# Performance work log

Hardware: AMD Instinct MI355X
Metric: run time of the kernel (lower is better)

Reference implementation:

```python
import jax, jax.numpy as jnp
import numpy as np

B, T, L, E, H, QS = 8, 8, 197, 768, 12, 16
C = E // H


def setup_inputs() -> dict:
    key = jax.random.key(0)
    ks = jax.random.split(key, 10)
    return dict(
        x=jax.random.normal(ks[0], (B, T, L, E), jnp.float32) * 0.02,
        s=jax.random.normal(ks[1], (B, QS, E), jnp.float32) * 0.02,
        te=jax.random.normal(ks[2], (T, E), jnp.float32) * 0.02,
        patch_mask=jax.random.normal(ks[3], (B, T, 1, L - 1, 1), jnp.float32) * 0.02,
        in_proj_weight=jax.random.normal(ks[4], (3 * E, E), jnp.float32) * 0.02,
        in_proj_bias=jax.random.normal(ks[5], (3 * E,), jnp.float32) * 0.02,
        out_w=jax.random.normal(ks[6], (E, E), jnp.float32) * 0.02,
        out_b=jax.random.normal(ks[7], (E,), jnp.float32) * 0.02,
        conv_w=jax.random.normal(ks[8], (E, 1, 3), jnp.float32) * 0.001,  # depthwise, groups=E
        conv_b=jax.random.normal(ks[9], (E,), jnp.float32) * 0.02,
    )


def _qkv(z, w, b, head_shape):
    # F.linear(z, w, b).chunk(3, -1), each reshaped to (*head_shape, H, C)
    zz = z @ w.T + b
    q, k, v = jnp.split(zz, 3, axis=-1)
    return (q.reshape(*head_shape, H, C),
            k.reshape(*head_shape, H, C),
            v.reshape(*head_shape, H, C))


def reference(x, s, te, patch_mask, in_proj_weight, in_proj_bias, out_w, out_b, conv_w, conv_b):
    scale = 1.0 / jnp.sqrt(jnp.asarray(C, x.dtype))

    # main self-attention over patches, per frame
    q, k, v = _qkv(x, in_proj_weight, in_proj_bias, (B, T, L))
    aff = jnp.einsum('ntqhc,ntkhc->ntqkh', q * scale, k)
    aff = jax.nn.softmax(aff, axis=-2)  # softmax over key dim (dim=-2)
    mix = jnp.einsum('ntqlh,ntlhc->ntqhc', aff, v)
    out = mix.reshape(B, T, L, E) @ out_w.T + out_b

    # syno cross-attention stream
    s_q, s_k, s_v = _qkv(s, in_proj_weight, in_proj_bias, (B, QS))
    te_q, te_k, te_v = _qkv(te, in_proj_weight, in_proj_bias, (T, 1))  # [T,1,H,C]
    _k = k[:, :, 1:]  # drop CLS -> [B,T,L-1,H,C]
    _v = v[:, :, 1:]
    s_aff = jnp.einsum('nqhc,ntkhc->ntqkh', s_q * scale, _k + te_k)
    s_aff = s_aff + patch_mask
    s_aff = jax.nn.softmax(s_aff, axis=-2)
    s_mix = jnp.einsum('ntqlh,ntlhc->ntqhc', s_aff, _v + te_v)  # [B,T,QS,H,C]

    # depthwise temporal conv (kernel 3, pad 1, groups=E) with residual
    sm = s_mix.transpose(0, 2, 3, 4, 1).reshape(B * QS, E, T)  # [N*Q, E, T]
    conv = jax.lax.conv_general_dilated(
        sm, conv_w, window_strides=(1,), padding=((1, 1),),
        feature_group_count=E, dimension_numbers=('NCH', 'OIH', 'NCH'))
    sm = conv + conv_b[None, :, None] + sm
    s_mix = sm.reshape(B, QS, H, C, T).transpose(0, 4, 1, 2, 3)  # [B,T,QS,H,C]

    s_mix = s_mix.mean(axis=1)  # mean over frames -> [B,QS,H,C]
    s_out = s_mix.reshape(B, QS, E) @ out_w.T + out_b

    return (q, k, v, out, s_q, s_k, s_v, s_out)
```

## Files before the change

kernel.cpp:

```cpp
#include <hip/hip_runtime.h>
#include <math.h>

constexpr int Bb  = 8;
constexpr int Tt  = 8;
constexpr int Ll  = 197;
constexpr int Ee  = 768;
constexpr int Hh  = 12;
constexpr int QSs = 16;
constexpr int Cc  = 64;
constexpr int MX    = Bb * Tt * Ll;
constexpr int MS    = Bb * QSs;
constexpr int MTE   = Tt;
constexpr int MPAD  = 12800;
constexpr int KkP = 224;

using f32x4 = __attribute__((ext_vector_type(4))) float;
using s16x8 = __attribute__((ext_vector_type(8))) short;

__device__ __forceinline__ unsigned short f2bf(float f) {
    unsigned int u = __float_as_uint(f);
    u = (u + 0x7fffu + ((u >> 16) & 1u)) >> 16;
    return (unsigned short)u;
}

__global__ __launch_bounds__(256) void convert_all(
    const float* __restrict__ x, const float* __restrict__ s,
    const float* __restrict__ te, const float* __restrict__ ipw,
    const float* __restrict__ ow, unsigned short* __restrict__ xb,
    unsigned short* __restrict__ wb, unsigned short* __restrict__ owb)
{
    const long oX  = (long)MX * Ee;
    const long oS  = oX + (long)MS * Ee;
    const long oTe = oS + (long)MTE * Ee;
    const long nXp = (long)MPAD * Ee;
    const long nW  = (long)3 * Ee * Ee;
    const long nOW = (long)Ee * Ee;
    const long i4 = ((long)blockIdx.x * 256 + threadIdx.x) * 4;

    const float* src = nullptr; unsigned short* dst; long off, soff = 0;
    if (i4 < nXp) {
        dst = xb; off = i4;
        if      (off < oX)  { src = x;  soff = off; }
        else if (off < oS)  { src = s;  soff = off - oX; }
        else if (off < oTe) { src = te; soff = off - oS; }
    } else if (i4 < nXp + nW) {
        dst = wb; off = i4 - nXp; src = ipw; soff = off;
    } else if (i4 < nXp + nW + nOW) {
        dst = owb; off = i4 - nXp - nW; src = ow; soff = off;
    } else return;

    float4 v = make_float4(0.f, 0.f, 0.f, 0.f);
    if (src) v = *reinterpret_cast<const float4*>(src + soff);
    ushort4 o;
    o.x = f2bf(v.x); o.y = f2bf(v.y); o.z = f2bf(v.z); o.w = f2bf(v.w);
    *reinterpret_cast<ushort4*>(dst + off) = o;
}

struct DstPtrs { float* d[9]; };

__device__ __forceinline__ void load_lds16(const unsigned short* g, unsigned short* l) {
    __builtin_amdgcn_global_load_lds(
        (const __attribute__((address_space(1))) unsigned int*)g,
        (__attribute__((address_space(3))) unsigned int*)l,
        16, 0, 0);
}

__global__ __launch_bounds__(1024, 4) void mfma_gemm256(
    const unsigned short* __restrict__ A,
    const unsigned short* __restrict__ W,
    const float* __restrict__ bias,
    DstPtrs dp, int Mmain, int Ms, int Mte,
    int ntiles, int tilesPerSeg)
{
    __shared__ __align__(16) unsigned short Asm[2][256 * 64];
    __shared__ __align__(16) unsigned short Bsm[2][256 * 64];

    const int nwg = gridDim.x;
    const int bid = blockIdx.x;
    const int q8 = nwg >> 3, r8 = nwg & 7;
    const int xcd = bid & 7, pos = bid >> 3;
    const int wgid = (xcd < r8 ? xcd * (q8 + 1)
                               : r8 * (q8 + 1) + (xcd - r8) * q8) + pos;
    const int mtile = wgid / ntiles;
    const int ntile = wgid - mtile * ntiles;

    const int tid  = threadIdx.x;
    const int wave = tid >> 6;
    const int lane = tid & 63;
    const int wm = wave >> 2;
    const int wn = wave & 3;
    const int m0  = mtile * 256;
    const int n0w = ntile * 256;
    const int seg = ntile / tilesPerSeg;
    const int n0g = (ntile % tilesPerSeg) * 256;

    const int frow = lane & 15;
    const int g    = lane >> 4;
    const int axr  = frow & 7;
    const int c0   = (g ^ axr) * 16;
    const int c1   = ((4 + g) ^ axr) * 16;

    f32x4 acc[4][4];
#pragma unroll
    for (int i = 0; i < 4; ++i)
#pragma unroll
        for (int j = 0; j < 4; ++j)
            acc[i][j] = f32x4{0.f, 0.f, 0.f, 0.f};

    const int srow = tid >> 3;
    const int scol = ((tid & 7) ^ ((tid >> 3) & 7)) * 8;
    const int sdst = tid * 8;

    const unsigned short* gA = A + (size_t)(m0 + srow) * 768 + scol;
    const unsigned short* gB = W + (size_t)(n0w + srow) * 768 + scol;

    auto STAGE_A = [&](int kt, int b) {
        const int k1 = kt * 64;
#pragma unroll
        for (int r = 0; r < 2; ++r)
            load_lds16(gA + (size_t)(r * 128) * 768 + k1,
                       &Asm[b][(r * 128) * 64 + sdst]);
    };
    auto STAGE_B = [&](int kt, int b) {
        const int k1 = kt * 64;
#pragma unroll
        for (int r = 0; r < 2; ++r)
            load_lds16(gB + (size_t)(r * 128) * 768 + k1,
                       &Bsm[b][(r * 128) * 64 + sdst]);
    };

    STAGE_A(0, 0);
    STAGE_B(0, 0);
    asm volatile("s_waitcnt vmcnt(0)" ::: "memory");
    __builtin_amdgcn_s_barrier();
    __builtin_amdgcn_sched_barrier(0);

    const int arow0 = wm * 64 + frow;
    const int brow0 = wn * 64 + frow;

    for (int kt = 0; kt < 12; ++kt) {
        const int cur = kt & 1;
        const char* As_ = (const char*)&Asm[cur][0];
        const char* Bs_ = (const char*)&Bsm[cur][0];
        const bool pre = kt < 11;

        s16x8 afr[4], bfr[4];
#pragma unroll
        for (int m = 0; m < 4; ++m)
            afr[m] = *reinterpret_cast<const s16x8*>(As_ + (arow0 + m * 16) * 128 + c0);
#pragma unroll
        for (int n = 0; n < 4; ++n)
            bfr[n] = *reinterpret_cast<const s16x8*>(Bs_ + (brow0 + n * 16) * 128 + c0);
        if (pre) { STAGE_A(kt + 1, cur ^ 1); STAGE_B(kt + 1, cur ^ 1); }
        asm volatile("s_waitcnt lgkmcnt(0)" ::: "memory");
        __builtin_amdgcn_sched_barrier(0);
        __builtin_amdgcn_s_setprio(1);
#pragma unroll
        for (int m = 0; m < 4; ++m)
#pragma unroll
            for (int n = 0; n < 4; ++n)
                acc[m][n] = __builtin_amdgcn_mfma_f32_16x16x32_bf16(
                    afr[m], bfr[n], acc[m][n], 0, 0, 0);
        __builtin_amdgcn_s_setprio(0);
#pragma unroll
        for (int m = 0; m < 4; ++m)
            afr[m] = *reinterpret_cast<const s16x8*>(As_ + (arow0 + m * 16) * 128 + c1);
#pragma unroll
        for (int n = 0; n < 4; ++n)
            bfr[n] = *reinterpret_cast<const s16x8*>(Bs_ + (brow0 + n * 16) * 128 + c1);
        asm volatile("s_waitcnt lgkmcnt(0)" ::: "memory");
        __builtin_amdgcn_sched_barrier(0);
        __builtin_amdgcn_s_setprio(1);
#pragma unroll
        for (int m = 0; m < 4; ++m)
#pragma unroll
            for (int n = 0; n < 4; ++n)
                acc[m][n] = __builtin_amdgcn_mfma_f32_16x16x32_bf16(
                    afr[m], bfr[n], acc[m][n], 0, 0, 0);
        __builtin_amdgcn_s_setprio(0);
        __builtin_amdgcn_sched_barrier(0);
        asm volatile("s_waitcnt vmcnt(0)" ::: "memory");
        __builtin_amdgcn_s_barrier();
        __builtin_amdgcn_sched_barrier(0);
    }

    {
        float* sc = (wave < 8 ? reinterpret_cast<float*>(&Asm[0][0])
                              : reinterpret_cast<float*>(&Bsm[0][0]))
                    + (wave & 7) * 1088;
        float bv[4];
#pragma unroll
        for (int n = 0; n < 4; ++n)
            bv[n] = bias[n0w + wn * 64 + n * 16 + frow];

        const int erow = lane >> 2;
        const int ecg  = lane & 3;

#pragma unroll
        for (int m = 0; m < 4; ++m) {
#pragma unroll
            for (int n = 0; n < 4; ++n)
#pragma unroll
                for (int r = 0; r < 4; ++r)
                    sc[(g * 4 + r) * 68 + n * 16 + frow] = acc[m][n][r] + bv[n];

            const int grow = m0 + wm * 64 + m * 16 + erow;
            float* base = nullptr; int lr = 0;
            if (grow < Mmain)                 { base = dp.d[seg];     lr = grow; }
            else if (grow < Mmain + Ms)       { base = dp.d[3 + seg]; lr = grow - Mmain; }
            else if (grow < Mmain + Ms + Mte) { base = dp.d[6 + seg]; lr = grow - Mmain - Ms; }
            if (base) {
                float* p = base + (size_t)lr * 768 + n0g + wn * 64 + ecg * 16;
                const float* sr = sc + erow * 68 + ecg * 16;
#pragma unroll
                for (int kq = 0; kq < 4; ++kq)
                    *reinterpret_cast<float4*>(p + kq * 4) =
                        *reinterpret_cast<const float4*>(sr + kq * 4);
            }
        }
    }
}

__global__ __launch_bounds__(256) void mfma_gemm(
    const unsigned short* __restrict__ A,
    const unsigned short* __restrict__ W,
    const float* __restrict__ bias,
    DstPtrs dp, int Mmain, int Ms, int Mte,
    int ntiles, int tilesPerSeg)
{
    __shared__ __align__(16) unsigned short Asm[2][128 * 32];
    __shared__ __align__(16) unsigned short Bsm[2][128 * 32];

    const int nwg = gridDim.x;
    const int bid = blockIdx.x;
    const int q8 = nwg >> 3, r8 = nwg & 7;
    const int xcd = bid & 7, pos = bid >> 3;
    const int wgid = (xcd < r8 ? xcd * (q8 + 1)
                               : r8 * (q8 + 1) + (xcd - r8) * q8) + pos;
    const int mtile = wgid / ntiles;
    const int ntile = wgid - mtile * ntiles;

    const int tid  = threadIdx.x;
    const int wave = tid >> 6;
    const int lane = tid & 63;
    const int wr = wave >> 1, wc = wave & 1;
    const int m0  = mtile * 128;
    const int seg = ntile / tilesPerSeg;
    const int n0g = (ntile % tilesPerSeg) * 128;
    const int n0w = ntile * 128;

    f32x4 acc[4][4];
#pragma unroll
    for (int i = 0; i < 4; ++i)
#pragma unroll
        for (int j = 0; j < 4; ++j)
            acc[i][j] = f32x4{0.f, 0.f, 0.f, 0.f};

    const int srow = tid >> 2;
    const int scol = (((tid & 3) ^ ((tid >> 3) & 3))) * 8;
    const int woff = wave * 512;

    const int frow = lane & 15;
    const int fkc  = ((lane >> 4) ^ ((frow >> 1) & 3)) * 8;

    const unsigned short* gA = A + (size_t)(m0 + srow) * 768 + scol;
    const unsigned short* gB = W + (size_t)(n0w + srow) * 768 + scol;

#pragma unroll
    for (int it = 0; it < 2; ++it) {
        load_lds16(gA + (size_t)it * 64 * 768, &Asm[0][woff + it * 2048]);
        load_lds16(gB + (size_t)it * 64 * 768, &Bsm[0][woff + it * 2048]);
    }
    asm volatile("s_waitcnt vmcnt(0)" ::: "memory");
    __syncthreads();

    for (int t = 0; t < 24; ++t) {
        const int cur = t & 1;
        if (t < 23) {
            const int k1 = (t + 1) * 32;
#pragma unroll
            for (int it = 0; it < 2; ++it) {
                load_lds16(gA + k1 + (size_t)it * 64 * 768, &Asm[cur ^ 1][woff + it * 2048]);
                load_lds16(gB + k1 + (size_t)it * 64 * 768, &Bsm[cur ^ 1][woff + it * 2048]);
            }
        }

        s16x8 af[4], bf[4];
#pragma unroll
        for (int i = 0; i < 4; ++i) {
            const int ar = wr * 64 + i * 16 + frow;
            af[i] = *reinterpret_cast<const s16x8*>(&Asm[cur][ar * 32 + fkc]);
        }
#pragma unroll
        for (int j = 0; j < 4; ++j) {
            const int br = wc * 64 + j * 16 + frow;
            bf[j] = *reinterpret_cast<const s16x8*>(&Bsm[cur][br * 32 + fkc]);
        }
#pragma unroll
        for (int i = 0; i < 4; ++i)
#pragma unroll
            for (int j = 0; j < 4; ++j)
                acc[i][j] = __builtin_amdgcn_mfma_f32_16x16x32_bf16(
                    af[i], bf[j], acc[i][j], 0, 0, 0);

        asm volatile("s_waitcnt vmcnt(0)" ::: "memory");
        __syncthreads();
    }

#pragma unroll
    for (int j = 0; j < 4; ++j) {
        const int col = wc * 64 + j * 16 + (lane & 15);
        const float bv = bias[n0w + col];
#pragma unroll
        for (int i = 0; i < 4; ++i) {
            const int gmBase = m0 + wr * 64 + i * 16 + ((lane >> 4) << 2);
            float* base; int lr;
            if (gmBase < Mmain)                { base = dp.d[seg];     lr = gmBase; }
            else if (gmBase < Mmain + Ms)      { base = dp.d[3 + seg]; lr = gmBase - Mmain; }
            else if (gmBase < Mmain + Ms + Mte){ base = dp.d[6 + seg]; lr = gmBase - Mmain - Ms; }
            else continue;
            float* p = base + (size_t)lr * 768 + n0g + col;
#pragma unroll
            for (int r = 0; r < 4; ++r)
                p[(size_t)r * 768] = acc[i][j][r] + bv;
        }
    }
}

__global__ __launch_bounds__(512, 2) void attn_mfma(
    const float* __restrict__ q, const float* __restrict__ k,
    const float* __restrict__ v, const float* __restrict__ sq,
    const float* __restrict__ tek, const float* __restrict__ tev,
    const float* __restrict__ pmask,
    unsigned short* __restrict__ mixb, float* __restrict__ smix)
{
    __shared__ __align__(16) unsigned short Ks[KkP * 64];
    __shared__ __align__(16) unsigned short Vt[64 * 256];
    __shared__ __align__(16) unsigned short Pb[8 * 16 * 256];
    __shared__ float pms[196];

    const int bidx = blockIdx.x;
    const int h  = bidx % Hh;
    const int bt = bidx / Hh;
    const int b  = bt / Tt;
    const int tt = bt % Tt;
    const int tid  = threadIdx.x;
    const int wave = tid >> 6;
    const int lane = tid & 63;
    const int l15  = lane & 15;
    const int g    = lane >> 4;
    const size_t gbase = (size_t)bt * Ll * Ee + (size_t)h * Cc;

    for (int idx = tid; idx < KkP * 16; idx += 512) {
        const int row = idx >> 4;
        const int cg  = idx & 15;
        float4 kv = make_float4(0.f, 0.f, 0.f, 0.f);
        if (row < Ll)
            kv = *reinterpret_cast<const float4*>(k + gbase + (size_t)row * Ee + cg * 4);
        ushort4 kb; kb.x = f2bf(kv.x); kb.y = f2bf(kv.y); kb.z = f2bf(kv.z); kb.w = f2bf(kv.w);
        const int kbyte = (row * 128 + cg * 8) ^ ((row & 7) << 4);
        *reinterpret_cast<ushort4*>((char*)Ks + kbyte) = kb;
    }
    for (int idx = tid; idx < 112 * 16; idx += 512) {
        const int rp = idx >> 4;
        const int cg = idx & 15;
        const int r0 = rp * 2, r1 = rp * 2 + 1;
        float4 v0 = make_float4(0.f, 0.f, 0.f, 0.f);
        float4 v1 = make_float4(0.f, 0.f, 0.f, 0.f);
        if (r0 < Ll) v0 = *reinterpret_cast<const float4*>(v + gbase + (size_t)r0 * Ee + cg * 4);
        if (r1 < Ll) v1 = *reinterpret_cast<const float4*>(v + gbase + (size_t)r1 * Ee + cg * 4);
        const float a0[4] = {v0.x, v0.y, v0.z, v0.w};
        const float a1[4] = {v1.x, v1.y, v1.z, v1.w};
#pragma unroll
        for (int i = 0; i < 4; ++i) {
            const int c = cg * 4 + i;
            const unsigned int w = (unsigned)f2bf(a0[i]) | ((unsigned)f2bf(a1[i]) << 16);
            const int vbyte = (c * 512 + rp * 4) ^ ((c & 7) << 4);
            *reinterpret_cast<unsigned int*>((char*)Vt + vbyte) = w;
        }
    }
    for (int i = tid; i < 196; i += 512)
        pms[i] = pmask[(size_t)bt * 196 + i];
    __syncthreads();

    char* Pw = (char*)(Pb + wave * 16 * 256);

    for (int qt = wave; qt < 14; qt += 8) {
        const bool stile = (qt == 13);
        s16x8 qf[2];
        float qte = 0.f;
        if (!stile) {
            const int qrow = qt * 16 + l15;
            const float* qp = q + gbase + (size_t)qrow * Ee;
#pragma unroll
            for (int ks = 0; ks < 2; ++ks) {
                float4 a = make_float4(0.f, 0.f, 0.f, 0.f);
                float4 c = make_float4(0.f, 0.f, 0.f, 0.f);
                if (qrow < Ll) {
                    a = *reinterpret_cast<const float4*>(qp + ks * 32 + g * 8);
                    c = *reinterpret_cast<const float4*>(qp + ks * 32 + g * 8 + 4);
                }
                qf[ks] = s16x8{(short)f2bf(a.x), (short)f2bf(a.y), (short)f2bf(a.z), (short)f2bf(a.w),
                               (short)f2bf(c.x), (short)f2bf(c.y), (short)f2bf(c.z), (short)f2bf(c.w)};
            }
        } else {
            const float* sp = sq + ((size_t)(b * QSs + l15)) * Ee + h * Cc;
            const float* tp = tek + (size_t)tt * Ee + h * Cc;
#pragma unroll
            for (int ks = 0; ks < 2; ++ks) {
                const float4 a = *reinterpret_cast<const float4*>(sp + ks * 32 + g * 8);
                const float4 c = *reinterpret_cast<const float4*>(sp + ks * 32 + g * 8 + 4);
                const float4 ta = *reinterpret_cast<const float4*>(tp + ks * 32 + g * 8);
                const float4 tc = *reinterpret_cast<const float4*>(tp + ks * 32 + g * 8 + 4);
                qf[ks] = s16x8{(short)f2bf(a.x), (short)f2bf(a.y), (short)f2bf(a.z), (short)f2bf(a.w),
                               (short)f2bf(c.x), (short)f2bf(c.y), (short)f2bf(c.z), (short)f2bf(c.w)};
                qte += a.x * ta.x + a.y * ta.y + a.z * ta.z + a.w * ta.w
                     + c.x * tc.x + c.y * tc.y + c.z * tc.z + c.w * tc.w;
            }
            qte += __shfl_xor(qte, 16);
            qte += __shfl_xor(qte, 32);
        }

        float lsq = 0.f;
        for (int kt = 0; kt < 14; ++kt) {
            const int krow = kt * 16 + l15;
            f32x4 acc = {0.f, 0.f, 0.f, 0.f};
#pragma unroll
            for (int ks = 0; ks < 2; ++ks) {
                const int byte = (krow * 128 + ks * 64 + g * 16) ^ ((krow & 7) << 4);
                const s16x8 kf = *reinterpret_cast<const s16x8*>((const char*)Ks + byte);
                acc = __builtin_amdgcn_mfma_f32_16x16x32_bf16(kf, qf[ks], acc, 0, 0, 0);
            }
            float p[4];
#pragma unroll
            for (int r = 0; r < 4; ++r) {
                const int kg = kt * 16 + g * 4 + r;
                float pv;
                if (!stile)
                    pv = (kg < Ll) ? __expf(acc[r] * 0.125f) : 0.f;
                else
                    pv = (kg >= 1 && kg < Ll)
                         ? __expf((acc[r] + qte) * 0.125f + pms[kg - 1]) : 0.f;
                p[r] = pv;
                lsq += pv;
            }
            const unsigned int w0 = (unsigned)f2bf(p[0]) | ((unsigned)f2bf(p[1]) << 16);
            const unsigned int w1 = (unsigned)f2bf(p[2]) | ((unsigned)f2bf(p[3]) << 16);
            const int k0 = kt * 16 + g * 4;
            const int pbyte = (l15 * 512 + k0 * 2) ^ ((l15 & 7) << 4);
            *reinterpret_cast<unsigned int*>(Pw + pbyte)     = w0;
            *reinterpret_cast<unsigned int*>(Pw + pbyte + 4) = w1;
        }
        lsq += __shfl_xor(lsq, 16);
        lsq += __shfl_xor(lsq, 32);
        const float invl = 1.f / lsq;

#pragma unroll
        for (int ct = 0; ct < 4; ++ct) {
            f32x4 acc = {0.f, 0.f, 0.f, 0.f};
#pragma unroll
            for (int ks = 0; ks < 7; ++ks) {
                const int pbyte = (l15 * 512 + ks * 64 + g * 16) ^ ((l15 & 7) << 4);
                const s16x8 pf = *reinterpret_cast<const s16x8*>(Pw + pbyte);
                const int crow = ct * 16 + l15;
                const int vbyte = (crow * 512 + ks * 64 + g * 16) ^ ((crow & 7) << 4);
                const s16x8 vf = *reinterpret_cast<const s16x8*>((const char*)Vt + vbyte);
                acc = __builtin_amdgcn_mfma_f32_16x16x32_bf16(pf, vf, acc, 0, 0, 0);
            }
#pragma unroll
            for (int r = 0; r < 4; ++r) {
                const int qw = g * 4 + r;
                const float iv = __shfl(invl, qw);
                if (!stile) {
                    const int qg = qt * 16 + qw;
                    if (qg < Ll)
                        mixb[(size_t)(bt * Ll + qg) * Ee + h * Cc + ct * 16 + l15] =
                            f2bf(acc[r] * iv);
                } else {
                    const int c = ct * 16 + l15;
                    const float tv = tev[(size_t)tt * Ee + h * Cc + c];
                    smix[((size_t)(bt * QSs + qw)) * Ee + h * Cc + c] =
                        acc[r] * iv + tv;
                }
            }
        }
    }
}

__global__ __launch_bounds__(256) void conv_mean_kernel(
    const float* __restrict__ smix, const float* __restrict__ cw,
    const float* __restrict__ cb, unsigned short* __restrict__ meansm_b)
{
    const int idx = blockIdx.x * 256 + threadIdx.x;
    if (idx >= Bb * QSs * Ee) return;
    const int e  = idx % Ee;
    const int n  = idx / Ee;
    const int b  = n / QSs;
    const int qi = n % QSs;

    float v0 = 0.f, vlast = 0.f, S = 0.f;
#pragma unroll
    for (int t = 0; t < Tt; ++t) {
        const float val = smix[((size_t)(b * Tt + t) * QSs + qi) * Ee + e];
        if (t == 0) v0 = val;
        if (t == Tt - 1) vlast = val;
        S += val;
    }
    const float w0 = cw[e * 3 + 0], w1 = cw[e * 3 + 1], w2 = cw[e * 3 + 2];
    const float tot = S + w0 * (S - vlast) + w1 * S + w2 * (S - v0);
    meansm_b[idx] = f2bf(tot * (1.f / Tt) + cb[e]);
}

extern "C" void kernel_launch(void* const* d_in, const int* in_sizes, int n_in,
                              void* d_out, int out_size, void* d_ws, size_t ws_size,
                              hipStream_t stream)
{
    const float* x     = (const float*)d_in[0];
    const float* s     = (const float*)d_in[1];
    const float* te    = (const float*)d_in[2];
    const float* pmask = (const float*)d_in[3];
    const float* ipw   = (const float*)d_in[4];
    const float* ipb   = (const float*)d_in[5];
    const float* ow    = (const float*)d_in[6];
    const float* ob    = (const float*)d_in[7];
    const float* cw    = (const float*)d_in[8];
    const float* cb    = (const float*)d_in[9];

    float* out = (float*)d_out;
    const size_t NX = (size_t)MX;
    float* q_o    = out;
    float* k_o    = q_o  + NX * Ee;
    float* v_o    = k_o  + NX * Ee;
    float* out_o  = v_o  + NX * Ee;
    float* sq_o   = out_o + NX * Ee;
    float* sk_o   = sq_o + (size_t)MS * Ee;
    float* sv_o   = sk_o + (size_t)MS * Ee;
    float* sout_o = sv_o + (size_t)MS * Ee;

    char* wsb = (char*)d_ws;
    unsigned short* xb   = (unsigned short*)wsb;
    unsigned short* wb   = xb + (size_t)MPAD * Ee;
    unsigned short* owb  = wb + (size_t)3 * Ee * Ee;
    unsigned short* meansm_b = owb + (size_t)Ee * Ee;
    float* teq    = (float*)(meansm_b + (size_t)MS * Ee);
    float* tek    = teq + (size_t)MTE * Ee;
    float* tev    = tek + (size_t)MTE * Ee;
    float* smix   = tev + (size_t)MTE * Ee;
    unsigned short* mixb = xb;

    const long nXp = (long)MPAD * Ee;
    const long nW  = (long)3 * Ee * Ee;
    const long nOW = (long)Ee * Ee;
    const long nCvt = (nXp + nW + nOW) / 4;

    convert_all<<<dim3((nCvt + 255) / 256), 256, 0, stream>>>(
        x, s, te, ipw, ow, xb, wb, owb);

    {
        DstPtrs dp;
        dp.d[0] = q_o;  dp.d[1] = k_o;  dp.d[2] = v_o;
        dp.d[3] = sq_o; dp.d[4] = sk_o; dp.d[5] = sv_o;
        dp.d[6] = teq;  dp.d[7] = tek;  dp.d[8] = tev;
        mfma_gemm256<<<dim3((MPAD / 256) * 9), 1024, 0, stream>>>(
            xb, wb, ipb, dp, MX, MS, MTE, 9, 3);
    }

    attn_mfma<<<dim3(Bb * Tt * Hh), 512, 0, stream>>>(
        q_o, k_o, v_o, sq_o, tek, tev, pmask, mixb, smix);

    {
        DstPtrs dp;
        for (int i = 0; i < 9; ++i) dp.d[i] = out_o;
        mfma_gemm256<<<dim3((MPAD / 256) * 3), 1024, 0, stream>>>(
            mixb, owb, ob, dp, MX, 0, 0, 3, 3);
    }

    conv_mean_kernel<<<dim3((Bb * QSs * Ee + 255) / 256), 256, 0, stream>>>(
        smix, cw, cb, meansm_b);

    {
        DstPtrs dp;
        for (int i = 0; i < 9; ++i) dp.d[i] = sout_o;
        mfma_gemm<<<dim3(6), 256, 0, stream>>>(
            meansm_b, owb, ob, dp, MS, 0, 0, 6, 6);
    }
}
```

Before: 219.8 us.

## Keep softmax probabilities in registers and feed PV MFMA directly

Drops the per-wave shared-memory staging buffer for the probability tile. Each 16x16 score accumulator is packed to bf16 and fed straight into 16x16x16 bf16 MFMAs against V, accumulating all four output column tiles in registers across key tiles. This removes the LDS write/read round trip and frees about 64KB of LDS so more blocks can fit per CU; launch bounds are raised to 4 blocks to match. In exchange it uses the smaller-K MFMA, which needs more instructions, and the tighter register budget implied by the launch bounds may cause spills.

```diff
diff --git a/kernel.cpp b/kernel.cpp
--- a/kernel.cpp
+++ b/kernel.cpp
@@ -16,6 +16,7 @@
 
 using f32x4 = __attribute__((ext_vector_type(4))) float;
 using s16x8 = __attribute__((ext_vector_type(8))) short;
+using s16x4 = __attribute__((ext_vector_type(4))) short;
 
 __device__ __forceinline__ unsigned short f2bf(float f) {
     unsigned int u = __float_as_uint(f);
@@ -327,7 +328,7 @@
     }
 }
 
-__global__ __launch_bounds__(512, 2) void attn_mfma(
+__global__ __launch_bounds__(512, 4) void attn_mfma(
     const float* __restrict__ q, const float* __restrict__ k,
     const float* __restrict__ v, const float* __restrict__ sq,
     const float* __restrict__ tek, const float* __restrict__ tev,
@@ -336,7 +337,6 @@
 {
     __shared__ __align__(16) unsigned short Ks[KkP * 64];
     __shared__ __align__(16) unsigned short Vt[64 * 256];
-    __shared__ __align__(16) unsigned short Pb[8 * 16 * 256];
     __shared__ float pms[196];
 
     const int bidx = blockIdx.x;
@@ -383,8 +383,6 @@
         pms[i] = pmask[(size_t)bt * 196 + i];
     __syncthreads();
 
-    char* Pw = (char*)(Pb + wave * 16 * 256);
-
     for (int qt = wave; qt < 14; qt += 8) {
         const bool stile = (qt == 13);
         s16x8 qf[2];
@@ -422,6 +420,10 @@
         }
 
         float lsq = 0.f;
+        f32x4 oacc[4];
+#pragma unroll
+        for (int ct = 0; ct < 4; ++ct) oacc[ct] = f32x4{0.f, 0.f, 0.f, 0.f};
+
         for (int kt = 0; kt < 14; ++kt) {
             const int krow = kt * 16 + l15;
             f32x4 acc = {0.f, 0.f, 0.f, 0.f};
@@ -444,12 +446,17 @@
                 p[r] = pv;
                 lsq += pv;
             }
-            const unsigned int w0 = (unsigned)f2bf(p[0]) | ((unsigned)f2bf(p[1]) << 16);
-            const unsigned int w1 = (unsigned)f2bf(p[2]) | ((unsigned)f2bf(p[3]) << 16);
-            const int k0 = kt * 16 + g * 4;
-            const int pbyte = (l15 * 512 + k0 * 2) ^ ((l15 & 7) << 4);
-            *reinterpret_cast<unsigned int*>(Pw + pbyte)     = w0;
-            *reinterpret_cast<unsigned int*>(Pw + pbyte + 4) = w1;
+            const s16x4 pa = s16x4{(short)f2bf(p[0]), (short)f2bf(p[1]),
+                                   (short)f2bf(p[2]), (short)f2bf(p[3])};
+            const int kb = (kt * 16 + g * 4) * 2;
+#pragma unroll
+            for (int ct = 0; ct < 4; ++ct) {
+                const int crow = ct * 16 + l15;
+                const int vbyte = (crow * 512 + kb) ^ ((crow & 7) << 4);
+                const s16x4 vb = *reinterpret_cast<const s16x4*>((const char*)Vt + vbyte);
+                oacc[ct] = __builtin_amdgcn_mfma_f32_16x16x16bf16_1k(
+                    pa, vb, oacc[ct], 0, 0, 0);
+            }
         }
         lsq += __shfl_xor(lsq, 16);
         lsq += __shfl_xor(lsq, 32);
@@ -457,16 +464,6 @@
 
 #pragma unroll
         for (int ct = 0; ct < 4; ++ct) {
-            f32x4 acc = {0.f, 0.f, 0.f, 0.f};
-#pragma unroll
-            for (int ks = 0; ks < 7; ++ks) {
-                const int pbyte = (l15 * 512 + ks * 64 + g * 16) ^ ((l15 & 7) << 4);
-                const s16x8 pf = *reinterpret_cast<const s16x8*>(Pw + pbyte);
-                const int crow = ct * 16 + l15;
-                const int vbyte = (crow * 512 + ks * 64 + g * 16) ^ ((crow & 7) << 4);
-                const s16x8 vf = *reinterpret_cast<const s16x8*>((const char*)Vt + vbyte);
-                acc = __builtin_amdgcn_mfma_f32_16x16x32_bf16(pf, vf, acc, 0, 0, 0);
-            }
 #pragma unroll
             for (int r = 0; r < 4; ++r) {
                 const int qw = g * 4 + r;
@@ -475,12 +472,12 @@
                     const int qg = qt * 16 + qw;
                     if (qg < Ll)
                         mixb[(size_t)(bt * Ll + qg) * Ee + h * Cc + ct * 16 + l15] =
-                            f2bf(acc[r] * iv);
+                            f2bf(oacc[ct][r] * iv);
                 } else {
                     const int c = ct * 16 + l15;
                     const float tv = tev[(size_t)tt * Ee + h * Cc + c];
                     smix[((size_t)(bt * QSs + qw)) * Ee + h * Cc + c] =
-                        acc[r] * iv + tv;
+                        oacc[ct][r] * iv + tv;
                 }
             }
         }
```

New measurement: 203.3 us, median of 2. 7.5% less time.
